# Optimization experiments

Hardware: AMD Instinct MI355X
Metric: run time of the kernel (lower is better)

The kernel has to match this reference:

```python
import jax, jax.numpy as jnp
import numpy as np

B = 2
SEQ = 384            # args.seq_len (per-stock sub-sequence length)
N_AUX = 4            # len(args.aux_tickers)
S = SEQ * N_AUX + 1  # global separator token + tiled sub-sequences
D_MODEL = 512
NHEAD = 8
HEAD_DIM = 64
ROPE = 32            # qk_rope_dim
KV_C = 256
Q_C = 384
D_FF = 1536
H2 = NHEAD * 2       # differential attention sub-heads
DH = HEAD_DIM // 2
RH = ROPE // 2
EPS = 1.1920929e-07  # torch RMSNorm default eps (fp32 machine eps)
SCALING = 1.0 / ((HEAD_DIM + ROPE) // 2)
LAMBDA_INIT = 0.8 - 0.6 * float(np.exp(-0.3 * 0))  # depth=0 -> 0.2


def rmsnorm(x, w, eps=EPS):
    return x * jax.lax.rsqrt(jnp.mean(jnp.square(x), -1, keepdims=True) + eps) * w


def apply_rope(xs, cos, sin):
    # xs: [B, N_AUX, SEQ, H2, RH]; cos/sin: [SEQ, RH//2]
    xr = xs[..., 0::2]
    xi = xs[..., 1::2]
    c = cos[None, None, :, None, :]
    s = sin[None, None, :, None, :]
    yr = xr * c - xi * s
    yi = xr * s + xi * c
    return jnp.stack([yr, yi], axis=-1).reshape(xs.shape)


def _build_mask():
    causal = np.triu(np.ones((SEQ, SEQ), np.bool_), 1)
    tiled = np.tile(causal, (N_AUX, N_AUX))
    m = np.ones((S, S), np.bool_)
    m[:, 0] = False          # everyone attends to global separator
    m[1:, 1:] = tiled
    return jnp.asarray(m)[None, None]  # [1,1,S,S], True = masked


MASK = _build_mask()


def setup_inputs() -> dict:
    key = jax.random.key(0)
    ks = jax.random.split(key, 16)

    def w(k, shape, std=0.02):
        return jax.random.normal(k, shape, jnp.float32) * std

    x = jax.random.normal(ks[0], (B, S, D_MODEL), jnp.float32)
    # rope table: complex [SEQ, ROPE//4] stored as (cos, sin)
    pairs = ROPE // 4
    inv = 1.0 / (10000.0 ** (np.arange(pairs, dtype=np.float64) / pairs))
    ang = np.outer(np.arange(SEQ), inv)
    freqs = jnp.asarray(np.stack([np.cos(ang), np.sin(ang)], -1), jnp.float32)
    return {
        'x': x,
        'freqs': freqs,
        'W_kv_down': w(ks[1], (D_MODEL, KV_C + ROPE)),
        'W_q_down': w(ks[2], (D_MODEL, Q_C)),
        'W_kv_up': w(ks[3], (KV_C, NHEAD * HEAD_DIM * 2)),
        'W_q_up': w(ks[4], (Q_C, NHEAD * (HEAD_DIM + ROPE))),
        'kv_norm_w': jnp.ones((KV_C,), jnp.float32),
        'q_norm_w': jnp.ones((Q_C,), jnp.float32),
        'W_o': w(ks[5], (NHEAD * HEAD_DIM, D_MODEL)),
        'lambda_q1': w(ks[6], (DH,), 0.1),
        'lambda_k1': w(ks[7], (DH,), 0.1),
        'lambda_q2': w(ks[8], (DH,), 0.1),
        'lambda_k2': w(ks[9], (DH,), 0.1),
        'head_norm_w': jnp.ones((HEAD_DIM,), jnp.float32),
        'norm1_w': jnp.ones((D_MODEL,), jnp.float32),
        'norm2_w': jnp.ones((D_MODEL,), jnp.float32),
        'W_ff_in': w(ks[10], (D_MODEL, 2 * D_FF)),
        'W_ff_out': w(ks[11], (D_FF, D_MODEL)),
    }


def reference(x, freqs, W_kv_down, W_q_down, W_kv_up, W_q_up, kv_norm_w, q_norm_w,
              W_o, lambda_q1, lambda_k1, lambda_q2, lambda_k2, head_norm_w,
              norm1_w, norm2_w, W_ff_in, W_ff_out):
    cos, sin = freqs[..., 0], freqs[..., 1]
    # ---- attention block (pre-norm) ----
    h = rmsnorm(x, norm1_w)
    ckv_full = h @ W_kv_down                               # [B,S,KV_C+ROPE]
    c_kv, k_rope = ckv_full[..., :KV_C], ckv_full[..., KV_C:]
    kv = (rmsnorm(c_kv, kv_norm_w) @ W_kv_up).reshape(B, S, NHEAD, 2 * HEAD_DIM)
    k, v = kv[..., :HEAD_DIM], kv[..., HEAD_DIM:]
    k = k.reshape(B, S, H2, DH)
    qf = (rmsnorm(h @ W_q_down, q_norm_w) @ W_q_up).reshape(B, S, NHEAD, HEAD_DIM + ROPE)
    q, q_rope = qf[..., :HEAD_DIM], qf[..., HEAD_DIM:]
    q = q.reshape(B, S, H2, DH)
    k_rope = jnp.broadcast_to(k_rope[:, :, None, :], (B, S, NHEAD, ROPE)).reshape(B, S, H2, RH)
    q_rope = q_rope.reshape(B, S, H2, RH)
    # split off global separator token, rope per sub-sequence
    q_sep, q_rot = q_rope[:, :1], q_rope[:, 1:].reshape(B, N_AUX, SEQ, H2, RH)
    k_sep, k_rot = k_rope[:, :1], k_rope[:, 1:].reshape(B, N_AUX, SEQ, H2, RH)
    q_rot = apply_rope(q_rot, cos, sin).reshape(B, S - 1, H2, RH)
    k_rot = apply_rope(k_rot, cos, sin).reshape(B, S - 1, H2, RH)
    q_rope = jnp.concatenate([q_sep, q_rot], axis=1)
    k_rope = jnp.concatenate([k_sep, k_rot], axis=1)
    qh = jnp.concatenate([q, q_rope], -1).transpose(0, 2, 1, 3)  # [B,H2,S,DH+RH]
    kh = jnp.concatenate([k, k_rope], -1).transpose(0, 2, 1, 3)
    a = jnp.einsum('bhqd,bhkd->bhqk', qh, kh) * SCALING
    abs_a = jnp.where(MASK, -1e9, jnp.abs(a))
    p = jnp.sign(a) * jax.nn.softmax(abs_a, axis=-1)
    lam = (jnp.exp(jnp.sum(lambda_q1 * lambda_k1)) -
           jnp.exp(jnp.sum(lambda_q2 * lambda_k2)) + LAMBDA_INIT)
    p = p.reshape(B, NHEAD, 2, S, S)
    G = jnp.mean(p[:, :, 0], axis=-1, keepdims=True)
    att = p[:, :, 0] - lam * p[:, :, 1] + G * lam
    att = jnp.where(MASK, 0.0, att)
    o = jnp.einsum('bhqk,bkhd->bqhd', att, v)              # [B,S,NHEAD,HEAD_DIM]
    o = rmsnorm(o, head_norm_w, 1e-5).reshape(B, S, NHEAD * HEAD_DIM)
    x = x + o @ W_o
    # ---- SwiGLU FFN ----
    h2 = rmsnorm(x, norm2_w)
    uv = h2 @ W_ff_in
    u, g = uv[..., :D_FF], uv[..., D_FF:]
    return x + (u * jax.nn.silu(g)) @ W_ff_out
```

## Files before the change

### kernel.cpp

```cpp
#include <hip/hip_runtime.h>

#define NB 2
#define SEQN 384
#define NS 1537
#define NS_PAD 1600
#define NH 8
#define H2N 16
#define NM (NB*NS)
#define DFF 1536
#define EPS1 1.1920929e-07f
#define SCAL (1.0f/48.0f)
#define SC2 (SCAL * 1.4426950408889634f)

#define SWZ(row, col) ((((row) << 6)) + ((col) ^ (((row) & 7) << 3)))

typedef __bf16 bf16x8 __attribute__((ext_vector_type(8)));
typedef _Float16 f16x8 __attribute__((ext_vector_type(8)));
typedef float f32x4 __attribute__((ext_vector_type(4)));

__device__ __forceinline__ unsigned short f2bf(float f) {
    unsigned int u = __builtin_bit_cast(unsigned int, f);
    u += 0x7FFFu + ((u >> 16) & 1u);
    return (unsigned short)(u >> 16);
}
__device__ __forceinline__ float bf2f(unsigned short h) {
    unsigned int u = ((unsigned int)h) << 16;
    return __builtin_bit_cast(float, u);
}

__host__ __device__ inline void tile_info(int t, int& nb0, int& nbc, int& w, int& nch) {
    int lo = (t == 0) ? 1 : t * 64;
    int hi0 = t * 64 + 63;
    int hi = hi0 < NS - 1 ? hi0 : NS - 1;
    int maxpos = ((lo - 1) / SEQN != (hi - 1) / SEQN) ? (SEQN - 1) : (hi - 1) % SEQN;
    nb0 = (maxpos + 65) >> 6;
    nbc = (maxpos + 64) >> 6;
    w = nb0 + 3 * nbc;
    nch = (w + 6) / 7;
}

struct TD { const float* w; unsigned short* hi; unsigned short* lo; int K; int N; int perm; };
struct TD7 { TD d[7]; int tend[7]; };

__global__ __launch_bounds__(256) void transpose_all(TD7 a) {
    __shared__ float tile[32][33];
    int t = blockIdx.x;
    int i = 0;
    while (t >= a.tend[i]) i++;
    int base = (i == 0) ? 0 : a.tend[i - 1];
    int lt = t - base;
    const float* w = a.d[i].w;
    unsigned short* hi = a.d[i].hi;
    unsigned short* lo = a.d[i].lo;
    int K = a.d[i].K, N = a.d[i].N, perm = a.d[i].perm;
    int Nh = N >> 1;
    int kt = (K + 31) / 32;
    int k0 = (lt % kt) * 32, n0 = (lt / kt) * 32;
    int tx = threadIdx.x & 31, ty4 = (threadIdx.x >> 5) * 4;
    for (int q = 0; q < 4; q++) {
        int k = k0 + ty4 + q, n = n0 + tx;
        tile[ty4 + q][tx] = (k < K && n < N) ? w[(size_t)k * N + n] : 0.f;
// ... 55 lines not shown
    float v0 = xx[288 + tid];
    float v1 = (tid < 128) ? xx[288 + 256 + tid] : 0.f;
    float ss2 = v0 * v0 + v1 * v1;
    for (int o = 1; o < 64; o <<= 1) ss2 += __shfl_xor(ss2, o);
    if ((tid & 63) == 0) red[tid >> 6] = ss2;
    __syncthreads();
    tot = red[0] + red[1] + red[2] + red[3];
    rs = rsqrtf(tot / 384.f + EPS1);
    float yb = v0 * rs * wB[tid];
    hb = f2bf(yb);
    bh_[(size_t)row * 384 + tid] = hb;
    bl_[(size_t)row * 384 + tid] = f2bf(yb - bf2f(hb));
    if (tid < 128) {
        float yc = v1 * rs * wB[256 + tid];
        unsigned short hc = f2bf(yc);
        bh_[(size_t)row * 384 + 256 + tid] = hc;
        bl_[(size_t)row * 384 + 256 + tid] = f2bf(yc - bf2f(hc));
    }
}

__global__ __launch_bounds__(256) void gemm_single(const unsigned short* __restrict__ A,
    const unsigned short* __restrict__ Bt, float* __restrict__ C_, const float* __restrict__ res,
    int M, int N, int K) {
    __shared__ unsigned short As[128][32];
    __shared__ unsigned short Bs[64][32];
    int m0 = blockIdx.x * 128, n0 = blockIdx.y * 64;
    int tid = threadIdx.x;
    int lane = tid & 63, wid = tid >> 6;
    int wr = wid >> 1, wc = wid & 1;
    int r = lane & 15, g = lane >> 4;
    int lrow = tid >> 2, lk = (tid & 3) * 8;
    f32x4 acc[4][2] = {};
    int ar0 = m0 + lrow, ar1 = m0 + 64 + lrow, brow = n0 + lrow;
    bool a0ok = ar0 < M, a1ok = ar1 < M, bok = brow < N;
    size_t a0off = (size_t)ar0 * K + lk, a1off = (size_t)ar1 * K + lk, boff = (size_t)brow * K + lk;
    for (int k0 = 0; k0 < K; k0 += 32) {
        uint4 av0 = {0,0,0,0}, av1 = {0,0,0,0}, bv = {0,0,0,0};
        if (a0ok) av0 = *(const uint4*)(A + a0off + k0);
        if (a1ok) av1 = *(const uint4*)(A + a1off + k0);
        if (bok)  bv  = *(const uint4*)(Bt + boff + k0);
        __syncthreads();
        *(uint4*)&As[lrow][lk] = av0;
        *(uint4*)&As[64 + lrow][lk] = av1;
        *(uint4*)&Bs[lrow][lk] = bv;
        __syncthreads();
        bf16x8 a[4], bb[2];
        #pragma unroll
        for (int i = 0; i < 4; i++) a[i] = *(const bf16x8*)&As[wr * 64 + i * 16 + r][g * 8];
        #pragma unroll
        for (int j = 0; j < 2; j++) bb[j] = *(const bf16x8*)&Bs[wc * 32 + j * 16 + r][g * 8];
        #pragma unroll
        for (int i = 0; i < 4; i++)
            #pragma unroll
            for (int j = 0; j < 2; j++)
                acc[i][j] = __builtin_amdgcn_mfma_f32_16x16x32_bf16(a[i], bb[j], acc[i][j], 0, 0, 0);
    }
    #pragma unroll
    for (int i = 0; i < 4; i++)
        #pragma unroll
        for (int j = 0; j < 2; j++) {
            int col = n0 + wc * 32 + j * 16 + r;
            if (col >= N) continue;
            #pragma unroll
            for (int e = 0; e < 4; e++) {
                int row = m0 + wr * 64 + i * 16 + g * 4 + e;
                if (row >= M) continue;
                float v = acc[i][j][e];
                if (res) v += res[(size_t)row * N + col];
                C_[(size_t)row * N + col] = v;
            }
        }
}

__global__ __launch_bounds__(256) void gemm_swiglu(const unsigned short* __restrict__ A,
    const unsigned short* __restrict__ Bt, unsigned short* __restrict__ act,
    int M, int N, int K) {
    __shared__ unsigned short As[128][32];
    __shared__ unsigned short Bs[64][32];
    int m0 = blockIdx.x * 128, n0 = blockIdx.y * 64;
    int tid = threadIdx.x;
    int lane = tid & 63, wid = tid >> 6;
    int wr = wid >> 1, wc = wid & 1;
    int r = lane & 15, g = lane >> 4;
    int lrow = tid >> 2, lk = (tid & 3) * 8;
    f32x4 acc[4][2] = {};
    int ar0 = m0 + lrow, ar1 = m0 + 64 + lrow, brow = n0 + lrow;
    bool a0ok = ar0 < M, a1ok = ar1 < M, bok = brow < N;
    size_t a0off = (size_t)ar0 * K + lk, a1off = (size_t)ar1 * K + lk, boff = (size_t)brow * K + lk;
    for (int k0 = 0; k0 < K; k0 += 32) {
        uint4 av0 = {0,0,0,0}, av1 = {0,0,0,0}, bv = {0,0,0,0};
        if (a0ok) av0 = *(const uint4*)(A + a0off + k0);
        if (a1ok) av1 = *(const uint4*)(A + a1off + k0);
        if (bok)  bv  = *(const uint4*)(Bt + boff + k0);
        __syncthreads();
        *(uint4*)&As[lrow][lk] = av0;
        *(uint4*)&As[64 + lrow][lk] = av1;
        *(uint4*)&Bs[lrow][lk] = bv;
        __syncthreads();
        bf16x8 a[4], bb[2];
        #pragma unroll
        for (int i = 0; i < 4; i++) a[i] = *(const bf16x8*)&As[wr * 64 + i * 16 + r][g * 8];
        #pragma unroll
        for (int j = 0; j < 2; j++) bb[j] = *(const bf16x8*)&Bs[wc * 32 + j * 16 + r][g * 8];
        #pragma unroll
        for (int i = 0; i < 4; i++)
            #pragma unroll
            for (int j = 0; j < 2; j++)
                acc[i][j] = __builtin_amdgcn_mfma_f32_16x16x32_bf16(a[i], bb[j], acc[i][j], 0, 0, 0);
    }
    int Nh = N >> 1;
    #pragma unroll
    for (int i = 0; i < 4; i++)
        #pragma unroll
        for (int j = 0; j < 2; j++) {
            int col = n0 + wc * 32 + j * 16 + r;
            #pragma unroll
            for (int e = 0; e < 4; e++) {
                int row = m0 + wr * 64 + i * 16 + g * 4 + e;
                float v = acc[i][j][e];
                float o = __shfl_xor(v, 1);
                if (((r & 1) == 0) && row < M && col < N) {
                    float u = v, gg = o;
                    float sg = gg / (1.f + __expf(-gg));
                    act[(size_t)row * Nh + (col >> 1)] = f2bf(u * sg);
                }
            }
        }
}

__global__ __launch_bounds__(256) void gemm_x3(const unsigned short* __restrict__ Ah,
    const unsigned short* __restrict__ Al, const unsigned short* __restrict__ Bh,
    const unsigned short* __restrict__ Bl, float* __restrict__ C_, int M, int N, int K) {
    __shared__ unsigned short AsH[128][32], AsL[128][32], BsH[64][32], BsL[64][32];
    int m0 = blockIdx.x * 128, n0 = blockIdx.y * 64;
    int tid = threadIdx.x;
    int lane = tid & 63, wid = tid >> 6;
    int wr = wid >> 1, wc = wid & 1;
    int r = lane & 15, g = lane >> 4;
    int lrow = tid >> 2, lk = (tid & 3) * 8;
    f32x4 acc[4][2] = {};
    int ar0 = m0 + lrow, ar1 = m0 + 64 + lrow, brow = n0 + lrow;
    bool a0ok = ar0 < M, a1ok = ar1 < M, bok = brow < N;
    size_t a0off = (size_t)ar0 * K + lk, a1off = (size_t)ar1 * K + lk, boff = (size_t)brow * K + lk;
    for (int k0 = 0; k0 < K; k0 += 32) {
        uint4 ah0 = {0,0,0,0}, al0 = {0,0,0,0}, ah1 = {0,0,0,0}, al1 = {0,0,0,0};
        uint4 bh0 = {0,0,0,0}, bl0 = {0,0,0,0};
        if (a0ok) { ah0 = *(const uint4*)(Ah + a0off + k0); al0 = *(const uint4*)(Al + a0off + k0); }
        if (a1ok) { ah1 = *(const uint4*)(Ah + a1off + k0); al1 = *(const uint4*)(Al + a1off + k0); }
        if (bok)  { bh0 = *(const uint4*)(Bh + boff + k0);  bl0 = *(const uint4*)(Bl + boff + k0); }
        __syncthreads();
        *(uint4*)&AsH[lrow][lk] = ah0; *(uint4*)&AsH[64 + lrow][lk] = ah1;
        *(uint4*)&AsL[lrow][lk] = al0; *(uint4*)&AsL[64 + lrow][lk] = al1;
        *(uint4*)&BsH[lrow][lk] = bh0; *(uint4*)&BsL[lrow][lk] = bl0;
        __syncthreads();
        bf16x8 ah[4], al[4], bh[2], bl[2];
        #pragma unroll
        for (int i = 0; i < 4; i++) {
            ah[i] = *(const bf16x8*)&AsH[wr * 64 + i * 16 + r][g * 8];
            al[i] = *(const bf16x8*)&AsL[wr * 64 + i * 16 + r][g * 8];
        }
        #pragma unroll
        for (int j = 0; j < 2; j++) {
            bh[j] = *(const bf16x8*)&BsH[wc * 32 + j * 16 + r][g * 8];
            bl[j] = *(const bf16x8*)&BsL[wc * 32 + j * 16 + r][g * 8];
        }
        #pragma unroll
        for (int i = 0; i < 4; i++)
            #pragma unroll
            for (int j = 0; j < 2; j++) {
                acc[i][j] = __builtin_amdgcn_mfma_f32_16x16x32_bf16(al[i], bh[j], acc[i][j], 0, 0, 0);
                acc[i][j] = __builtin_amdgcn_mfma_f32_16x16x32_bf16(ah[i], bl[j], acc[i][j], 0, 0, 0);
                acc[i][j] = __builtin_amdgcn_mfma_f32_16x16x32_bf16(ah[i], bh[j], acc[i][j], 0, 0, 0);
            }
    }
    #pragma unroll
    for (int i = 0; i < 4; i++)
        #pragma unroll
        for (int j = 0; j < 2; j++) {
            int col = n0 + wc * 32 + j * 16 + r;
            if (col >= N) continue;
            #pragma unroll
            for (int e = 0; e < 4; e++) {
                int row = m0 + wr * 64 + i * 16 + g * 4 + e;
                if (row < M) C_[(size_t)row * N + col] = acc[i][j][e];
            }
        }
}

__global__ void assemble2(const float* __restrict__ qf_, const float* __restrict__ kvf,
    const float* __restrict__ cq, const float* __restrict__ freqs,
    _Float16* __restrict__ qgh, _Float16* __restrict__ qgl,
    _Float16* __restrict__ kgh, _Float16* __restrict__ kgl) {
    size_t idx = (size_t)blockIdx.x * 256 + threadIdx.x;
    const size_t total = (size_t)NB * H2N * NS_PAD * 32;
    if (idx >= total) return;
    int j2 = (int)(idx & 31);
// ... 58 lines not shown
    int bh = blockIdx.x; int b = bh >> 3, h = bh & 7;
    int d = threadIdx.x & 63, ps = threadIdx.x >> 6;
    int p0 = ps * 96;
    float run = 0.f;
    for (int i = 0; i < 96; i++) {
        int p = p0 + i;
        float s = 0.f;
        #pragma unroll
        for (int c = 0; c < 4; c++)
            s += kvf[((size_t)(b * NS + 1 + c * SEQN + p)) * 1024 + h * 128 + 64 + d];
        run += s;
        P4[((size_t)bh * SEQN + p) * 64 + d] = run;
    }
    tot[ps][d] = run;
    __syncthreads();
    if (ps > 0) {
        float off = 0.f;
        for (int j = 0; j < ps; j++) off += tot[j][d];
        for (int i = 0; i < 96; i++)
            P4[((size_t)bh * SEQN + p0 + i) * 64 + d] += off;
    }
}

struct FlashTab { int4 e[80]; };

__global__ __launch_bounds__(256) void flash_chunk(
    const _Float16* __restrict__ qgh, const _Float16* __restrict__ qgl,
    const _Float16* __restrict__ kgh, const _Float16* __restrict__ kgl,
    const _Float16* __restrict__ vt,
    float* __restrict__ Opart, float* __restrict__ zpart, FlashTab tab) {
    __shared__ _Float16 Ksh[2][64 * 64];
    __shared__ _Float16 Ksl[2][64 * 64];
    __shared__ _Float16 Vt[64 * 64];
    __shared__ _Float16 Pl[4][16 * 64];
    const int4 E = tab.e[blockIdx.x];
    const int tq = E.x, kti0 = E.y, nk = E.z, slot = E.w;
    const int bh = blockIdx.y;
    const int b = bh >> 3, h = bh & 7;
    const int qs0 = tq * 64;
    const int tid = threadIdx.x;
    const int wave = tid >> 6, lane = tid & 63;
    const int r = lane & 15, g = lane >> 4;
    const int qrow = qs0 + wave * 16;
    const size_t sh0 = (size_t)(bh * 2);

    int nb0, nbc, w_, nch_;
    tile_info(tq, nb0, nbc, w_, nch_);

    f16x8 qfh[2][2], qfl[2][2];
    #pragma unroll
    for (int sub = 0; sub < 2; sub++)
        #pragma unroll
        for (int ks = 0; ks < 2; ks++) {
            size_t off = ((sh0 + sub) * NS_PAD + qrow + r) * 64 + ks * 32 + g * 8;
            qfh[sub][ks] = *(const f16x8*)(qgh + off);
            qfl[sub][ks] = *(const f16x8*)(qgl + off);
        }

    float z0p[4] = {0.f,0.f,0.f,0.f}, g0p[4] = {0.f,0.f,0.f,0.f}, z1p[4] = {0.f,0.f,0.f,0.f};
    f32x4 O0[4], O1[4];
    #pragma unroll
    for (int e = 0; e < 4; e++) { O0[e] = (f32x4){0.f,0.f,0.f,0.f}; O1[e] = (f32x4){0.f,0.f,0.f,0.f}; }
    int qpos[4];
    #pragma unroll
    for (int e = 0; e < 4; e++) {
        int q = qrow + g * 4 + e;
        qpos[e] = (q == 0) ? -1 : (q - 1) % SEQN;
    }

    for (int ii = 0; ii < nk; ii++) {
        int kti = kti0 + ii;
        int c, j;
        if (kti < nb0) { c = 0; j = kti; }
        else { int m = kti - nb0; c = 1 + m / nbc; j = m - (c - 1) * nbc; }
        int kbase = (c == 0) ? j * 64 : c * SEQN + 1 + j * 64;
        int cbase = c * SEQN + 1;
        __syncthreads();
        #pragma unroll
        for (int i = 0; i < 4; i++) {
            int chunk = i * 256 + tid;
            int arr = chunk >> 9;
            int cc = chunk & 511;
            int row = cc >> 3, c8 = (cc & 7) * 8;
            size_t goff = ((sh0 + arr) * NS_PAD + kbase + row) * 64 + c8;
            int di = SWZ(row, c8);
            *(uint4*)&Ksh[arr][di] = *(const uint4*)(kgh + goff);
            *(uint4*)&Ksl[arr][di] = *(const uint4*)(kgl + goff);
        }
        #pragma unroll
        for (int i = 0; i < 2; i++) {
            int cc = i * 256 + tid;
            int d = cc >> 3, c8 = (cc & 7) * 8;
            *(uint4*)&Vt[SWZ(d, c8)] =
                *(const uint4*)(vt + ((size_t)(bh * 64 + d)) * NS_PAD + kbase + c8);
        }
        __syncthreads();

        f16x8 bv[4][2];
        #pragma unroll
        for (int dt = 0; dt < 4; dt++)
            #pragma unroll
            for (int ks = 0; ks < 2; ks++)
                bv[dt][ks] = *(const f16x8*)&Vt[SWZ(dt * 16 + r, ks * 32 + g * 8)];

        bool um[4][4];
        #pragma unroll
        for (int t4 = 0; t4 < 4; t4++) {
            int kk2 = kbase + t4 * 16 + r;
            int rel = kk2 - cbase;
            #pragma unroll
            for (int e = 0; e < 4; e++)
                um[e][t4] = (kk2 == 0) ||
                            ((unsigned)rel < (unsigned)SEQN && rel <= qpos[e]);
        }

        #pragma unroll
        for (int sub = 0; sub < 2; sub++) {
            f32x4 acc[4];
            #pragma unroll
            for (int t4 = 0; t4 < 4; t4++) acc[t4] = (f32x4){0.f,0.f,0.f,0.f};
            #pragma unroll
            for (int t4 = 0; t4 < 4; t4++)
                #pragma unroll
                for (int ks = 0; ks < 2; ks++) {
                    int ki = SWZ(t4 * 16 + r, ks * 32 + g * 8);
                    f16x8 bkh = *(const f16x8*)&Ksh[sub][ki];
                    f16x8 bkl = *(const f16x8*)&Ksl[sub][ki];
                    acc[t4] = __builtin_amdgcn_mfma_f32_16x16x32_f16(qfl[sub][ks], bkh, acc[t4], 0, 0, 0);
                    acc[t4] = __builtin_amdgcn_mfma_f32_16x16x32_f16(qfh[sub][ks], bkl, acc[t4], 0, 0, 0);
                    acc[t4] = __builtin_amdgcn_mfma_f32_16x16x32_f16(qfh[sub][ks], bkh, acc[t4], 0, 0, 0);
                }
            #pragma unroll
            for (int e = 0; e < 4; e++) {
                #pragma unroll
                for (int t4 = 0; t4 < 4; t4++) {
                    float a = acc[t4][e];
                    float ef = exp2f(fabsf(a) * SC2);
                    float ev = um[e][t4] ? ef : 0.f;
                    float pvv = copysignf(ev, a);
                    if (sub == 0) { z0p[e] += ev; g0p[e] += pvv; }
                    else          { z1p[e] += ev; }
                    Pl[wave][SWZ(g * 4 + e, t4 * 16 + r)] = (_Float16)pvv;
                }
            }
            __builtin_amdgcn_wave_barrier();
            f16x8 pa0 = *(const f16x8*)&Pl[wave][SWZ(r, g * 8)];
            f16x8 pa1 = *(const f16x8*)&Pl[wave][SWZ(r, 32 + g * 8)];
            #pragma unroll
            for (int dt = 0; dt < 4; dt++) {
                if (sub == 0) {
                    O0[dt] = __builtin_amdgcn_mfma_f32_16x16x32_f16(pa0, bv[dt][0], O0[dt], 0, 0, 0);
                    O0[dt] = __builtin_amdgcn_mfma_f32_16x16x32_f16(pa1, bv[dt][1], O0[dt], 0, 0, 0);
                } else {
                    O1[dt] = __builtin_amdgcn_mfma_f32_16x16x32_f16(pa0, bv[dt][0], O1[dt], 0, 0, 0);
                    O1[dt] = __builtin_amdgcn_mfma_f32_16x16x32_f16(pa1, bv[dt][1], O1[dt], 0, 0, 0);
                }
            }
        }
    }

    #pragma unroll
    for (int e = 0; e < 4; e++) {
        float z0 = z0p[e], g0 = g0p[e], z1 = z1p[e];
        #pragma unroll
        for (int o = 1; o < 16; o <<= 1) {
            z0 += __shfl_xor(z0, o); g0 += __shfl_xor(g0, o); z1 += __shfl_xor(z1, o);
        }
        int q = qrow + g * 4 + e;
        if (q < NS) {
            if (r == 0) {
                float* zp = zpart + (((size_t)slot * 16 + bh) * NS + q) * 4;
                zp[0] = z0; zp[1] = g0; zp[2] = z1;
            }
            float* op = Opart + (((size_t)slot * 16 + bh) * NS + q) * 128;
            #pragma unroll
            for (int dt = 0; dt < 4; dt++) {
                op[dt * 16 + r] = O0[dt][e];
                op[64 + dt * 16 + r] = O1[dt][e];
            }
        }
    }
}

__global__ __launch_bounds__(256) void combine_attn(const float* __restrict__ Opart,
    const float* __restrict__ zpart, const float* __restrict__ kvf,
    const float* __restrict__ P4,
    const float* __restrict__ lq1, const float* __restrict__ lk1,
    const float* __restrict__ lq2, const float* __restrict__ lk2,
    const float* __restrict__ hw, unsigned short* __restrict__ o_n) {
    __shared__ float lamS;
    if (threadIdx.x < 32) {
        float p1 = lq1[threadIdx.x] * lk1[threadIdx.x];
        float p2 = lq2[threadIdx.x] * lk2[threadIdx.x];
        for (int o = 1; o < 32; o <<= 1) { p1 += __shfl_xor(p1, o); p2 += __shfl_xor(p2, o); }
        if (threadIdx.x == 0) lamS = expf(p1) - expf(p2) + 0.2f;
    }
    __syncthreads();
    float lam = lamS;
    int b = blockIdx.z, h = blockIdx.y, bh = b * 8 + h;
    int ql = threadIdx.x >> 2, dp = threadIdx.x & 3;
    int q = blockIdx.x * 64 + ql;
    bool ok = q < NS;
    int qc = ok ? q : 0;
    int tq = qc >> 6;
    int nb0_, nbc_, w_, nch;
    tile_info(tq, nb0_, nbc_, w_, nch);
    float z0 = 0.f, g0 = 0.f, z1 = 0.f;
    float O0a[16], O1a[16];
    #pragma unroll
    for (int i = 0; i < 16; i++) { O0a[i] = 0.f; O1a[i] = 0.f; }
    for (int s = 0; s < nch; s++) {
        size_t ib = ((size_t)s * 16 + bh) * NS + qc;
        const float* zp = zpart + ib * 4;
        z0 += zp[0]; g0 += zp[1]; z1 += zp[2];
        const float* op = Opart + ib * 128 + dp * 16;
        #pragma unroll
        for (int i = 0; i < 16; i++) { O0a[i] += op[i]; O1a[i] += op[64 + i]; }
    }
    float iz0 = 1.f / z0;
    float l1 = lam / z1;
    float Gl = lam * g0 * iz0 * (1.f / (float)NS);
    int qpos = (q == 0) ? -1 : (q - 1) % SEQN;
    float of[16]; float ss = 0.f;
    #pragma unroll
    for (int i = 0; i < 16; i++) {
        int d = dp * 16 + i;
        float vs = kvf[((size_t)(b * NS)) * 1024 + h * 128 + 64 + d];
        if (qpos >= 0) vs += P4[((size_t)bh * SEQN + qpos) * 64 + d];
        float o = O0a[i] * iz0 - O1a[i] * l1 + Gl * vs;
        of[i] = o; ss += o * o;
    }
    ss += __shfl_xor(ss, 1); ss += __shfl_xor(ss, 2);
    float rs = rsqrtf(ss / 64.f + 1e-5f);
    if (ok) {
        unsigned int pk[8];
        #pragma unroll
        for (int i = 0; i < 8; i++) {
            unsigned int a = f2bf(of[2 * i] * rs * hw[dp * 16 + 2 * i]);
            unsigned int c = f2bf(of[2 * i + 1] * rs * hw[dp * 16 + 2 * i + 1]);
            pk[i] = a | (c << 16);
        }
        unsigned short* dst = o_n + ((size_t)(b * NS + q)) * 512 + h * 64 + dp * 16;
        *(uint4*)dst = *(uint4*)&pk[0];
        *(uint4*)(dst + 8) = *(uint4*)&pk[4];
    }
}

extern "C" void kernel_launch(void* const* d_in, const int* in_sizes, int n_in,
                              void* d_out, int out_size, void* d_ws, size_t ws_size,
                              hipStream_t stream) {
    (void)in_sizes; (void)n_in; (void)out_size; (void)ws_size;
    const float* x    = (const float*)d_in[0];
// ... 30 lines not shown
    unsigned short* wffi_h = (unsigned short*)alloc((size_t)512 * 3072 * 2);
    unsigned short* wffo_h = (unsigned short*)alloc((size_t)1536 * 512 * 2);
    unsigned short* h_hi   = (unsigned short*)alloc((size_t)NM * 512 * 2);
    unsigned short* h_lo   = (unsigned short*)alloc((size_t)NM * 512 * 2);
    char* cq0 = p;
    float* cq = (float*)alloc((size_t)NM * 672 * 4);
    float* x2 = (float*)cq0;
    char* nb0_ = p;
    unsigned short* ckvn_h = (unsigned short*)alloc((size_t)NM * 256 * 2);
    unsigned short* ckvn_l = (unsigned short*)alloc((size_t)NM * 256 * 2);
    unsigned short* qdn_h  = (unsigned short*)alloc((size_t)NM * 384 * 2);
    unsigned short* qdn_l  = (unsigned short*)alloc((size_t)NM * 384 * 2);
    unsigned short* o_n    = (unsigned short*)alloc((size_t)NM * 512 * 2);
    unsigned short* h2     = (unsigned short*)alloc((size_t)NM * 512 * 2);
    unsigned short* act    = (unsigned short*)nb0_;
    float* kvf = (float*)alloc((size_t)NM * 1024 * 4);
    float* qff = (float*)alloc((size_t)NM * 768 * 4);
    _Float16* qgh = (_Float16*)alloc((size_t)NB * H2N * NS_PAD * 64 * 2);
    _Float16* qgl = (_Float16*)alloc((size_t)NB * H2N * NS_PAD * 64 * 2);
    _Float16* kgh = (_Float16*)alloc((size_t)NB * H2N * NS_PAD * 64 * 2);
    _Float16* kgl = (_Float16*)alloc((size_t)NB * H2N * NS_PAD * 64 * 2);
    _Float16* vt  = (_Float16*)alloc((size_t)NB * NH * 64 * NS_PAD * 2);
    float* P4     = (float*)alloc((size_t)NB * NH * SEQN * 64 * 4);
    float* Opart  = (float*)alloc((size_t)4 * 16 * NS * 128 * 4);
    float* zpart  = (float*)alloc((size_t)4 * 16 * NS * 4 * 4);

    int cum = 0;
    {
        TD7 a;
        const float* ws_[7] = {Wkvd, Wqd, Wkvu, Wqu, Wo, Wffi, Wffo};
        unsigned short* his[7] = {wcq_h, wcq_h + (size_t)288 * 512, wkvu_h, wqu_h, wo_h, wffi_h, wffo_h};
        unsigned short* los[7] = {wcq_l, wcq_l + (size_t)288 * 512, wkvu_l, wqu_l, nullptr, nullptr, nullptr};
        int Ks[7] = {512, 512, 256, 384, 512, 512, 1536};
        int Ns[7] = {288, 384, 1024, 768, 512, 3072, 512};
        int pm[7] = {0, 0, 0, 0, 0, 1, 0};
        for (int i = 0; i < 7; i++) {
            a.d[i] = TD{ws_[i], his[i], los[i], Ks[i], Ns[i], pm[i]};
            cum += ((Ks[i] + 31) / 32) * ((Ns[i] + 31) / 32);
            a.tend[i] = cum;
        }
        transpose_all<<<dim3(cum), 256, 0, stream>>>(a);
    }

    rmsnorm_k<<<NM, 256, 0, stream>>>(x, n1w, h_hi, h_lo, 512, 512, EPS1);

    const int GX = (NM + 127) / 128;
    gemm_x3<<<dim3(GX, (672 + 63) / 64), 256, 0, stream>>>(h_hi, h_lo, wcq_h, wcq_l, cq, NM, 672, 512);

    rmsnorm_dual<<<NM, 256, 0, stream>>>(cq, kvnw, qnw, ckvn_h, ckvn_l, qdn_h, qdn_l);

    gemm_x3<<<dim3(GX, 1024 / 64), 256, 0, stream>>>(ckvn_h, ckvn_l, wkvu_h, wkvu_l, kvf, NM, 1024, 256);
    gemm_x3<<<dim3(GX, 768 / 64), 256, 0, stream>>>(qdn_h, qdn_l, wqu_h, wqu_l, qff, NM, 768, 384);

    {
        size_t total = (size_t)NB * H2N * NS_PAD * 32;
        assemble2<<<dim3((unsigned)((total + 255) / 256)), 256, 0, stream>>>(
            qff, kvf, cq, freqs, qgh, qgl, kgh, kgl);
    }
    vtrans<<<dim3(NS_PAD / 64, NB * NH), 256, 0, stream>>>(kvf, vt);
    prefix2_k<<<dim3(NB * NH), 256, 0, stream>>>(kvf, P4);

    {
        FlashTab tab;
        int ne = 0;
        for (int t = 0; t < (NS + 63) / 64; t++) {
            int nb0c, nbcc, w, nch;
            tile_info(t, nb0c, nbcc, w, nch);
            int base = 0;
            for (int i = 0; i < nch; i++) {
                int sz = w / nch + (i < w % nch ? 1 : 0);
                tab.e[ne++] = make_int4(t, base, sz, i);
                base += sz;
            }
        }
        for (int i = 1; i < ne; i++) {
            int4 key = tab.e[i];
            int j = i - 1;
            while (j >= 0 && tab.e[j].z < key.z) { tab.e[j + 1] = tab.e[j]; j--; }
            tab.e[j + 1] = key;
        }
        flash_chunk<<<dim3(ne, 16), 256, 0, stream>>>(qgh, qgl, kgh, kgl, vt, Opart, zpart, tab);
    }
    combine_attn<<<dim3((NS + 63) / 64, NH, NB), 256, 0, stream>>>(
        Opart, zpart, kvf, P4, lq1, lk1, lq2, lk2, hnw, o_n);

    gemm_single<<<dim3(GX, 512 / 64), 256, 0, stream>>>(o_n, wo_h, x2, x, NM, 512, 512);
    rmsnorm_k<<<NM, 256, 0, stream>>>(x2, n2w, h2, nullptr, 512, 512, EPS1);
    gemm_swiglu<<<dim3(GX, 3072 / 64), 256, 0, stream>>>(h2, wffi_h, act, NM, 3072, 512);
    gemm_single<<<dim3(GX, 512 / 64), 256, 0, stream>>>(act, wffo_h, out, x2, NM, 512, 1536);
}
```

Before: 311.7 us.

## Widen GEMM K-tiles with swizzled LDS and replace chunked flash table with fixed 2-way split

All three GEMM kernels now stage 64-wide K slices in XOR-swizzled shared memory instead of 32-wide padded-free arrays. This halves the number of barrier pairs per K loop and avoids LDS bank conflicts. The attention kernel drops the host-built work table of load-balanced chunks in favour of a fixed split into two halves over the four sub-sequences, adding s_setprio around the MFMA blocks. The combine kernel now sums exactly two partials. The fixed split may balance load worse than the sorted chunk table, and the bigger tiles use more LDS, which can lower occupancy.

```diff
diff --git a/kernel.cpp b/kernel.cpp
--- a/kernel.cpp
+++ b/kernel.cpp
@@ -26,17 +26,6 @@
 __device__ __forceinline__ float bf2f(unsigned short h) {
     unsigned int u = ((unsigned int)h) << 16;
     return __builtin_bit_cast(float, u);
-}
-
-__host__ __device__ inline void tile_info(int t, int& nb0, int& nbc, int& w, int& nch) {
-    int lo = (t == 0) ? 1 : t * 64;
-    int hi0 = t * 64 + 63;
-    int hi = hi0 < NS - 1 ? hi0 : NS - 1;
-    int maxpos = ((lo - 1) / SEQN != (hi - 1) / SEQN) ? (SEQN - 1) : (hi - 1) % SEQN;
-    nb0 = (maxpos + 65) >> 6;
-    nbc = (maxpos + 64) >> 6;
-    w = nb0 + 3 * nbc;
-    nch = (w + 6) / 7;
 }
 
 struct TD { const float* w; unsigned short* hi; unsigned short* lo; int K; int N; int perm; };
@@ -138,38 +127,54 @@
 __global__ __launch_bounds__(256) void gemm_single(const unsigned short* __restrict__ A,
     const unsigned short* __restrict__ Bt, float* __restrict__ C_, const float* __restrict__ res,
     int M, int N, int K) {
-    __shared__ unsigned short As[128][32];
-    __shared__ unsigned short Bs[64][32];
+    __shared__ unsigned short As[128 * 64];
+    __shared__ unsigned short Bs[64 * 64];
     int m0 = blockIdx.x * 128, n0 = blockIdx.y * 64;
     int tid = threadIdx.x;
     int lane = tid & 63, wid = tid >> 6;
     int wr = wid >> 1, wc = wid & 1;
     int r = lane & 15, g = lane >> 4;
-    int lrow = tid >> 2, lk = (tid & 3) * 8;
+    int lrow = tid >> 3, lk = (tid & 7) * 8;
     f32x4 acc[4][2] = {};
-    int ar0 = m0 + lrow, ar1 = m0 + 64 + lrow, brow = n0 + lrow;
-    bool a0ok = ar0 < M, a1ok = ar1 < M, bok = brow < N;
-    size_t a0off = (size_t)ar0 * K + lk, a1off = (size_t)ar1 * K + lk, boff = (size_t)brow * K + lk;
-    for (int k0 = 0; k0 < K; k0 += 32) {
-        uint4 av0 = {0,0,0,0}, av1 = {0,0,0,0}, bv = {0,0,0,0};
-        if (a0ok) av0 = *(const uint4*)(A + a0off + k0);
-        if (a1ok) av1 = *(const uint4*)(A + a1off + k0);
-        if (bok)  bv  = *(const uint4*)(Bt + boff + k0);
+    bool aok[4]; size_t aoff[4];
+    #pragma unroll
+    for (int p = 0; p < 4; p++) {
+        int ar = m0 + p * 32 + lrow;
+        aok[p] = ar < M;
+        aoff[p] = (size_t)ar * K + lk;
+    }
+    bool bok[2]; size_t boff[2];
+    #pragma unroll
+    for (int p = 0; p < 2; p++) {
+        int br = n0 + p * 32 + lrow;
+        bok[p] = br < N;
+        boff[p] = (size_t)br * K + lk;
+    }
+    for (int k0 = 0; k0 < K; k0 += 64) {
+        uint4 av[4], bv[2];
+        #pragma unroll
+        for (int p = 0; p < 4; p++) av[p] = aok[p] ? *(const uint4*)(A + aoff[p] + k0) : (uint4){0,0,0,0};
+        #pragma unroll
+        for (int p = 0; p < 2; p++) bv[p] = bok[p] ? *(const uint4*)(Bt + boff[p] + k0) : (uint4){0,0,0,0};
         __syncthreads();
-        *(uint4*)&As[lrow][lk] = av0;
-        *(uint4*)&As[64 + lrow][lk] = av1;
-        *(uint4*)&Bs[lrow][lk] = bv;
+        #pragma unroll
+        for (int p = 0; p < 4; p++) *(uint4*)&As[SWZ(p * 32 + lrow, lk)] = av[p];
+        #pragma unroll
+        for (int p = 0; p < 2; p++) *(uint4*)&Bs[SWZ(p * 32 + lrow, lk)] = bv[p];
         __syncthreads();
-        bf16x8 a[4], bb[2];
-        #pragma unroll
-        for (int i = 0; i < 4; i++) a[i] = *(const bf16x8*)&As[wr * 64 + i * 16 + r][g * 8];
-        #pragma unroll
-        for (int j = 0; j < 2; j++) bb[j] = *(const bf16x8*)&Bs[wc * 32 + j * 16 + r][g * 8];
-        #pragma unroll
-        for (int i = 0; i < 4; i++)
-            #pragma unroll
-            for (int j = 0; j < 2; j++)
-                acc[i][j] = __builtin_amdgcn_mfma_f32_16x16x32_bf16(a[i], bb[j], acc[i][j], 0, 0, 0);
+        #pragma unroll
+        for (int ks = 0; ks < 2; ks++) {
+            bf16x8 a[4], bb[2];
+            #pragma unroll
+            for (int i = 0; i < 4; i++) a[i] = *(const bf16x8*)&As[SWZ(wr * 64 + i * 16 + r, ks * 32 + g * 8)];
+            #pragma unroll
+            for (int j = 0; j < 2; j++) bb[j] = *(const bf16x8*)&Bs[SWZ(wc * 32 + j * 16 + r, ks * 32 + g * 8)];
+            #pragma unroll
+            for (int i = 0; i < 4; i++)
+                #pragma unroll
+                for (int j = 0; j < 2; j++)
+                    acc[i][j] = __builtin_amdgcn_mfma_f32_16x16x32_bf16(a[i], bb[j], acc[i][j], 0, 0, 0);
+        }
     }
     #pragma unroll
     for (int i = 0; i < 4; i++)
@@ -191,38 +196,54 @@
 __global__ __launch_bounds__(256) void gemm_swiglu(const unsigned short* __restrict__ A,
     const unsigned short* __restrict__ Bt, unsigned short* __restrict__ act,
     int M, int N, int K) {
-    __shared__ unsigned short As[128][32];
-    __shared__ unsigned short Bs[64][32];
+    __shared__ unsigned short As[128 * 64];
+    __shared__ unsigned short Bs[64 * 64];
     int m0 = blockIdx.x * 128, n0 = blockIdx.y * 64;
     int tid = threadIdx.x;
     int lane = tid & 63, wid = tid >> 6;
     int wr = wid >> 1, wc = wid & 1;
     int r = lane & 15, g = lane >> 4;
-    int lrow = tid >> 2, lk = (tid & 3) * 8;
+    int lrow = tid >> 3, lk = (tid & 7) * 8;
     f32x4 acc[4][2] = {};
-    int ar0 = m0 + lrow, ar1 = m0 + 64 + lrow, brow = n0 + lrow;
-    bool a0ok = ar0 < M, a1ok = ar1 < M, bok = brow < N;
-    size_t a0off = (size_t)ar0 * K + lk, a1off = (size_t)ar1 * K + lk, boff = (size_t)brow * K + lk;
-    for (int k0 = 0; k0 < K; k0 += 32) {
-        uint4 av0 = {0,0,0,0}, av1 = {0,0,0,0}, bv = {0,0,0,0};
-        if (a0ok) av0 = *(const uint4*)(A + a0off + k0);
-        if (a1ok) av1 = *(const uint4*)(A + a1off + k0);
-        if (bok)  bv  = *(const uint4*)(Bt + boff + k0);
+    bool aok[4]; size_t aoff[4];
+    #pragma unroll
+    for (int p = 0; p < 4; p++) {
+        int ar = m0 + p * 32 + lrow;
+        aok[p] = ar < M;
+        aoff[p] = (size_t)ar * K + lk;
+    }
+    bool bok[2]; size_t boff[2];
+    #pragma unroll
+    for (int p = 0; p < 2; p++) {
+        int br = n0 + p * 32 + lrow;
+        bok[p] = br < N;
+        boff[p] = (size_t)br * K + lk;
+    }
+    for (int k0 = 0; k0 < K; k0 += 64) {
+        uint4 av[4], bv[2];
+        #pragma unroll
+        for (int p = 0; p < 4; p++) av[p] = aok[p] ? *(const uint4*)(A + aoff[p] + k0) : (uint4){0,0,0,0};
+        #pragma unroll
+        for (int p = 0; p < 2; p++) bv[p] = bok[p] ? *(const uint4*)(Bt + boff[p] + k0) : (uint4){0,0,0,0};
         __syncthreads();
-        *(uint4*)&As[lrow][lk] = av0;
-        *(uint4*)&As[64 + lrow][lk] = av1;
-        *(uint4*)&Bs[lrow][lk] = bv;
+        #pragma unroll
+        for (int p = 0; p < 4; p++) *(uint4*)&As[SWZ(p * 32 + lrow, lk)] = av[p];
+        #pragma unroll
+        for (int p = 0; p < 2; p++) *(uint4*)&Bs[SWZ(p * 32 + lrow, lk)] = bv[p];
         __syncthreads();
-        bf16x8 a[4], bb[2];
-        #pragma unroll
-        for (int i = 0; i < 4; i++) a[i] = *(const bf16x8*)&As[wr * 64 + i * 16 + r][g * 8];
-        #pragma unroll
-        for (int j = 0; j < 2; j++) bb[j] = *(const bf16x8*)&Bs[wc * 32 + j * 16 + r][g * 8];
-        #pragma unroll
-        for (int i = 0; i < 4; i++)
-            #pragma unroll
-            for (int j = 0; j < 2; j++)
-                acc[i][j] = __builtin_amdgcn_mfma_f32_16x16x32_bf16(a[i], bb[j], acc[i][j], 0, 0, 0);
+        #pragma unroll
+        for (int ks = 0; ks < 2; ks++) {
+            bf16x8 a[4], bb[2];
+            #pragma unroll
+            for (int i = 0; i < 4; i++) a[i] = *(const bf16x8*)&As[SWZ(wr * 64 + i * 16 + r, ks * 32 + g * 8)];
+            #pragma unroll
+            for (int j = 0; j < 2; j++) bb[j] = *(const bf16x8*)&Bs[SWZ(wc * 32 + j * 16 + r, ks * 32 + g * 8)];
+            #pragma unroll
+            for (int i = 0; i < 4; i++)
+                #pragma unroll
+                for (int j = 0; j < 2; j++)
+                    acc[i][j] = __builtin_amdgcn_mfma_f32_16x16x32_bf16(a[i], bb[j], acc[i][j], 0, 0, 0);
+        }
     }
     int Nh = N >> 1;
     #pragma unroll
@@ -247,47 +268,76 @@
 __global__ __launch_bounds__(256) void gemm_x3(const unsigned short* __restrict__ Ah,
     const unsigned short* __restrict__ Al, const unsigned short* __restrict__ Bh,
     const unsigned short* __restrict__ Bl, float* __restrict__ C_, int M, int N, int K) {
-    __shared__ unsigned short AsH[128][32], AsL[128][32], BsH[64][32], BsL[64][32];
+    __shared__ unsigned short AsH[128 * 64], AsL[128 * 64], BsH[64 * 64], BsL[64 * 64];
     int m0 = blockIdx.x * 128, n0 = blockIdx.y * 64;
     int tid = threadIdx.x;
     int lane = tid & 63, wid = tid >> 6;
     int wr = wid >> 1, wc = wid & 1;
     int r = lane & 15, g = lane >> 4;
-    int lrow = tid >> 2, lk = (tid & 3) * 8;
+    int lrow = tid >> 3, lk = (tid & 7) * 8;
     f32x4 acc[4][2] = {};
-    int ar0 = m0 + lrow, ar1 = m0 + 64 + lrow, brow = n0 + lrow;
-    bool a0ok = ar0 < M, a1ok = ar1 < M, bok = brow < N;
-    size_t a0off = (size_t)ar0 * K + lk, a1off = (size_t)ar1 * K + lk, boff = (size_t)brow * K + lk;
-    for (int k0 = 0; k0 < K; k0 += 32) {
-        uint4 ah0 = {0,0,0,0}, al0 = {0,0,0,0}, ah1 = {0,0,0,0}, al1 = {0,0,0,0};
-        uint4 bh0 = {0,0,0,0}, bl0 = {0,0,0,0};
-        if (a0ok) { ah0 = *(const uint4*)(Ah + a0off + k0); al0 = *(const uint4*)(Al + a0off + k0); }
-        if (a1ok) { ah1 = *(const uint4*)(Ah + a1off + k0); al1 = *(const uint4*)(Al + a1off + k0); }
-        if (bok)  { bh0 = *(const uint4*)(Bh + boff + k0);  bl0 = *(const uint4*)(Bl + boff + k0); }
+    bool aok[4]; size_t aoff[4];
+    #pragma unroll
+    for (int p = 0; p < 4; p++) {
+        int ar = m0 + p * 32 + lrow;
+        aok[p] = ar < M;
+        aoff[p] = (size_t)ar * K + lk;
+    }
+    bool bok[2]; size_t boff[2];
+    #pragma unroll
+    for (int p = 0; p < 2; p++) {
+        int br = n0 + p * 32 + lrow;
+        bok[p] = br < N;
+        boff[p] = (size_t)br * K + lk;
+    }
+    for (int k0 = 0; k0 < K; k0 += 64) {
+        uint4 avh[4], avl[4], bvh[2], bvl[2];
+        #pragma unroll
+        for (int p = 0; p < 4; p++) {
+            avh[p] = aok[p] ? *(const uint4*)(Ah + aoff[p] + k0) : (uint4){0,0,0,0};
+            avl[p] = aok[p] ? *(const uint4*)(Al + aoff[p] + k0) : (uint4){0,0,0,0};
+        }
+        #pragma unroll
+        for (int p = 0; p < 2; p++) {
+            bvh[p] = bok[p] ? *(const uint4*)(Bh + boff[p] + k0) : (uint4){0,0,0,0};
+            bvl[p] = bok[p] ? *(const uint4*)(Bl + boff[p] + k0) : (uint4){0,0,0,0};
+        }
         __syncthreads();
-        *(uint4*)&AsH[lrow][lk] = ah0; *(uint4*)&AsH[64 + lrow][lk] = ah1;
-        *(uint4*)&AsL[lrow][lk] = al0; *(uint4*)&AsL[64 + lrow][lk] = al1;
-        *(uint4*)&BsH[lrow][lk] = bh0; *(uint4*)&BsL[lrow][lk] = bl0;
+        #pragma unroll
+        for (int p = 0; p < 4; p++) {
+            *(uint4*)&AsH[SWZ(p * 32 + lrow, lk)] = avh[p];
+            *(uint4*)&AsL[SWZ(p * 32 + lrow, lk)] = avl[p];
+        }
+        #pragma unroll
+        for (int p = 0; p < 2; p++) {
+            *(uint4*)&BsH[SWZ(p * 32 + lrow, lk)] = bvh[p];
+            *(uint4*)&BsL[SWZ(p * 32 + lrow, lk)] = bvl[p];
+        }
         __syncthreads();
-        bf16x8 ah[4], al[4], bh[2], bl[2];
-        #pragma unroll
-        for (int i = 0; i < 4; i++) {
-            ah[i] = *(const bf16x8*)&AsH[wr * 64 + i * 16 + r][g * 8];
-            al[i] = *(const bf16x8*)&AsL[wr * 64 + i * 16 + r][g * 8];
-        }
-        #pragma unroll
-        for (int j = 0; j < 2; j++) {
-            bh[j] = *(const bf16x8*)&BsH[wc * 32 + j * 16 + r][g * 8];
-            bl[j] = *(const bf16x8*)&BsL[wc * 32 + j * 16 + r][g * 8];
-        }
-        #pragma unroll
-        for (int i = 0; i < 4; i++)
+        #pragma unroll
+        for (int ks = 0; ks < 2; ks++) {
+            bf16x8 ah[4], al[4], bh[2], bl[2];
+            #pragma unroll
+            for (int i = 0; i < 4; i++) {
+                int ai = SWZ(wr * 64 + i * 16 + r, ks * 32 + g * 8);
+                ah[i] = *(const bf16x8*)&AsH[ai];
+                al[i] = *(const bf16x8*)&AsL[ai];
+            }
             #pragma unroll
             for (int j = 0; j < 2; j++) {
-                acc[i][j] = __builtin_amdgcn_mfma_f32_16x16x32_bf16(al[i], bh[j], acc[i][j], 0, 0, 0);
-                acc[i][j] = __builtin_amdgcn_mfma_f32_16x16x32_bf16(ah[i], bl[j], acc[i][j], 0, 0, 0);
-                acc[i][j] = __builtin_amdgcn_mfma_f32_16x16x32_bf16(ah[i], bh[j], acc[i][j], 0, 0, 0);
-            }
+                int bi = SWZ(wc * 32 + j * 16 + r, ks * 32 + g * 8);
+                bh[j] = *(const bf16x8*)&BsH[bi];
+                bl[j] = *(const bf16x8*)&BsL[bi];
+            }
+            #pragma unroll
+            for (int i = 0; i < 4; i++)
+                #pragma unroll
+                for (int j = 0; j < 2; j++) {
+                    acc[i][j] = __builtin_amdgcn_mfma_f32_16x16x32_bf16(al[i], bh[j], acc[i][j], 0, 0, 0);
+                    acc[i][j] = __builtin_amdgcn_mfma_f32_16x16x32_bf16(ah[i], bl[j], acc[i][j], 0, 0, 0);
+                    acc[i][j] = __builtin_amdgcn_mfma_f32_16x16x32_bf16(ah[i], bh[j], acc[i][j], 0, 0, 0);
+                }
+        }
     }
     #pragma unroll
     for (int i = 0; i < 4; i++)
@@ -392,31 +442,26 @@
     }
 }
 
-struct FlashTab { int4 e[80]; };
-
-__global__ __launch_bounds__(256) void flash_chunk(
+__global__ __launch_bounds__(256) void flash_split(
     const _Float16* __restrict__ qgh, const _Float16* __restrict__ qgl,
     const _Float16* __restrict__ kgh, const _Float16* __restrict__ kgl,
     const _Float16* __restrict__ vt,
-    float* __restrict__ Opart, float* __restrict__ zpart, FlashTab tab) {
+    float* __restrict__ Opart, float* __restrict__ zpart) {
     __shared__ _Float16 Ksh[2][64 * 64];
     __shared__ _Float16 Ksl[2][64 * 64];
     __shared__ _Float16 Vt[64 * 64];
     __shared__ _Float16 Pl[4][16 * 64];
-    const int4 E = tab.e[blockIdx.x];
-    const int tq = E.x, kti0 = E.y, nk = E.z, slot = E.w;
-    const int bh = blockIdx.y;
-    const int b = bh >> 3, h = bh & 7;
-    const int qs0 = tq * 64;
+    const int tile = blockIdx.x;
+    const int h = blockIdx.y & 7, split = blockIdx.y >> 3;
+    const int b = blockIdx.z;
+    const int bh = b * 8 + h;
+    const int qs0 = tile * 64;
     const int tid = threadIdx.x;
     const int wave = tid >> 6, lane = tid & 63;
     const int r = lane & 15, g = lane >> 4;
     const int qrow = qs0 + wave * 16;
     const size_t sh0 = (size_t)(bh * 2);
 
-    int nb0, nbc, w_, nch_;
-    tile_info(tq, nb0, nbc, w_, nch_);
-
     f16x8 qfh[2][2], qfl[2][2];
     #pragma unroll
     for (int sub = 0; sub < 2; sub++)
@@ -437,94 +482,101 @@
         int q = qrow + g * 4 + e;
         qpos[e] = (q == 0) ? -1 : (q - 1) % SEQN;
     }
-
-    for (int ii = 0; ii < nk; ii++) {
-        int kti = kti0 + ii;
-        int c, j;
-        if (kti < nb0) { c = 0; j = kti; }
-        else { int m = kti - nb0; c = 1 + m / nbc; j = m - (c - 1) * nbc; }
-        int kbase = (c == 0) ? j * 64 : c * SEQN + 1 + j * 64;
+    int lo = qs0 < 1 ? 1 : qs0;
+    int hi = qs0 + 63 < NS - 1 ? qs0 + 63 : NS - 1;
+    int maxpos = ((lo - 1) / SEQN != (hi - 1) / SEQN) ? (SEQN - 1) : (hi - 1) % SEQN;
+
+    for (int c = 2 * split; c < 2 * split + 2; c++) {
+        int nb = (c == 0) ? ((maxpos + 2 + 63) >> 6) : ((maxpos + 1 + 63) >> 6);
+        int kstart = (c == 0) ? 0 : (c * SEQN + 1);
         int cbase = c * SEQN + 1;
-        __syncthreads();
-        #pragma unroll
-        for (int i = 0; i < 4; i++) {
-            int chunk = i * 256 + tid;
-            int arr = chunk >> 9;
-            int cc = chunk & 511;
-            int row = cc >> 3, c8 = (cc & 7) * 8;
-            size_t goff = ((sh0 + arr) * NS_PAD + kbase + row) * 64 + c8;
-            int di = SWZ(row, c8);
-            *(uint4*)&Ksh[arr][di] = *(const uint4*)(kgh + goff);
-            *(uint4*)&Ksl[arr][di] = *(const uint4*)(kgl + goff);
-        }
-        #pragma unroll
-        for (int i = 0; i < 2; i++) {
-            int cc = i * 256 + tid;
-            int d = cc >> 3, c8 = (cc & 7) * 8;
-            *(uint4*)&Vt[SWZ(d, c8)] =
-                *(const uint4*)(vt + ((size_t)(bh * 64 + d)) * NS_PAD + kbase + c8);
-        }
-        __syncthreads();
-
-        f16x8 bv[4][2];
-        #pragma unroll
-        for (int dt = 0; dt < 4; dt++)
-            #pragma unroll
-            for (int ks = 0; ks < 2; ks++)
-                bv[dt][ks] = *(const f16x8*)&Vt[SWZ(dt * 16 + r, ks * 32 + g * 8)];
-
-        bool um[4][4];
-        #pragma unroll
-        for (int t4 = 0; t4 < 4; t4++) {
-            int kk2 = kbase + t4 * 16 + r;
-            int rel = kk2 - cbase;
-            #pragma unroll
-            for (int e = 0; e < 4; e++)
-                um[e][t4] = (kk2 == 0) ||
-                            ((unsigned)rel < (unsigned)SEQN && rel <= qpos[e]);
-        }
-
-        #pragma unroll
-        for (int sub = 0; sub < 2; sub++) {
-            f32x4 acc[4];
-            #pragma unroll
-            for (int t4 = 0; t4 < 4; t4++) acc[t4] = (f32x4){0.f,0.f,0.f,0.f};
-            #pragma unroll
-            for (int t4 = 0; t4 < 4; t4++)
-                #pragma unroll
-                for (int ks = 0; ks < 2; ks++) {
-                    int ki = SWZ(t4 * 16 + r, ks * 32 + g * 8);
-                    f16x8 bkh = *(const f16x8*)&Ksh[sub][ki];
-                    f16x8 bkl = *(const f16x8*)&Ksl[sub][ki];
-                    acc[t4] = __builtin_amdgcn_mfma_f32_16x16x32_f16(qfl[sub][ks], bkh, acc[t4], 0, 0, 0);
-                    acc[t4] = __builtin_amdgcn_mfma_f32_16x16x32_f16(qfh[sub][ks], bkl, acc[t4], 0, 0, 0);
-                    acc[t4] = __builtin_amdgcn_mfma_f32_16x16x32_f16(qfh[sub][ks], bkh, acc[t4], 0, 0, 0);
+        for (int j = 0; j < nb; j++) {
+            int kbase = kstart + j * 64;
+            __syncthreads();
+            #pragma unroll
+            for (int i = 0; i < 4; i++) {
+                int chunk = i * 256 + tid;
+                int arr = chunk >> 9;
+                int cc = chunk & 511;
+                int row = cc >> 3, c8 = (cc & 7) * 8;
+                size_t goff = ((sh0 + arr) * NS_PAD + kbase + row) * 64 + c8;
+                int di = SWZ(row, c8);
+                *(uint4*)&Ksh[arr][di] = *(const uint4*)(kgh + goff);
+                *(uint4*)&Ksl[arr][di] = *(const uint4*)(kgl + goff);
+            }
+            #pragma unroll
+            for (int i = 0; i < 2; i++) {
+                int cc = i * 256 + tid;
+                int d = cc >> 3, c8 = (cc & 7) * 8;
+                *(uint4*)&Vt[SWZ(d, c8)] =
+                    *(const uint4*)(vt + ((size_t)(bh * 64 + d)) * NS_PAD + kbase + c8);
+            }
+            __syncthreads();
+
+            f16x8 bv[4][2];
+            #pragma unroll
+            for (int dt = 0; dt < 4; dt++)
+                #pragma unroll
+                for (int ks = 0; ks < 2; ks++)
+                    bv[dt][ks] = *(const f16x8*)&Vt[SWZ(dt * 16 + r, ks * 32 + g * 8)];
+
+            bool um[4][4];
+            #pragma unroll
+            for (int t4 = 0; t4 < 4; t4++) {
+                int kk2 = kbase + t4 * 16 + r;
+                int rel = kk2 - cbase;
+                #pragma unroll
+                for (int e = 0; e < 4; e++)
+                    um[e][t4] = (kk2 == 0) ||
+                                ((unsigned)rel < (unsigned)SEQN && rel <= qpos[e]);
+            }
+
+            #pragma unroll
+            for (int sub = 0; sub < 2; sub++) {
+                f32x4 acc[4];
+                #pragma unroll
+                for (int t4 = 0; t4 < 4; t4++) acc[t4] = (f32x4){0.f,0.f,0.f,0.f};
+                __builtin_amdgcn_s_setprio(1);
+                #pragma unroll
+                for (int t4 = 0; t4 < 4; t4++)
+                    #pragma unroll
+                    for (int ks = 0; ks < 2; ks++) {
+                        int ki = SWZ(t4 * 16 + r, ks * 32 + g * 8);
+                        f16x8 bkh = *(const f16x8*)&Ksh[sub][ki];
+                        f16x8 bkl = *(const f16x8*)&Ksl[sub][ki];
+                        acc[t4] = __builtin_amdgcn_mfma_f32_16x16x32_f16(qfl[sub][ks], bkh, acc[t4], 0, 0, 0);
+                        acc[t4] = __builtin_amdgcn_mfma_f32_16x16x32_f16(qfh[sub][ks], bkl, acc[t4], 0, 0, 0);
+                        acc[t4] = __builtin_amdgcn_mfma_f32_16x16x32_f16(qfh[sub][ks], bkh, acc[t4], 0, 0, 0);
+                    }
+                __builtin_amdgcn_s_setprio(0);
+                #pragma unroll
+                for (int e = 0; e < 4; e++) {
+                    #pragma unroll
+                    for (int t4 = 0; t4 < 4; t4++) {
+                        float a = acc[t4][e];
+                        float ef = exp2f(fabsf(a) * SC2);
+                        float ev = um[e][t4] ? ef : 0.f;
+                        float pvv = copysignf(ev, a);
+                        if (sub == 0) { z0p[e] += ev; g0p[e] += pvv; }
+                        else          { z1p[e] += ev; }
+                        Pl[wave][SWZ(g * 4 + e, t4 * 16 + r)] = (_Float16)pvv;
+                    }
                 }
-            #pragma unroll
-            for (int e = 0; e < 4; e++) {
-                #pragma unroll
-                for (int t4 = 0; t4 < 4; t4++) {
-                    float a = acc[t4][e];
-                    float ef = exp2f(fabsf(a) * SC2);
-                    float ev = um[e][t4] ? ef : 0.f;
-                    float pvv = copysignf(ev, a);
-                    if (sub == 0) { z0p[e] += ev; g0p[e] += pvv; }
-                    else          { z1p[e] += ev; }
-                    Pl[wave][SWZ(g * 4 + e, t4 * 16 + r)] = (_Float16)pvv;
+                __builtin_amdgcn_wave_barrier();
+                f16x8 pa0 = *(const f16x8*)&Pl[wave][SWZ(r, g * 8)];
+                f16x8 pa1 = *(const f16x8*)&Pl[wave][SWZ(r, 32 + g * 8)];
+                __builtin_amdgcn_s_setprio(1);
+                #pragma unroll
+                for (int dt = 0; dt < 4; dt++) {
+                    if (sub == 0) {
+                        O0[dt] = __builtin_amdgcn_mfma_f32_16x16x32_f16(pa0, bv[dt][0], O0[dt], 0, 0, 0);
+                        O0[dt] = __builtin_amdgcn_mfma_f32_16x16x32_f16(pa1, bv[dt][1], O0[dt], 0, 0, 0);
+                    } else {
+                        O1[dt] = __builtin_amdgcn_mfma_f32_16x16x32_f16(pa0, bv[dt][0], O1[dt], 0, 0, 0);
+                        O1[dt] = __builtin_amdgcn_mfma_f32_16x16x32_f16(pa1, bv[dt][1], O1[dt], 0, 0, 0);
+                    }
                 }
-            }
-            __builtin_amdgcn_wave_barrier();
-            f16x8 pa0 = *(const f16x8*)&Pl[wave][SWZ(r, g * 8)];
-            f16x8 pa1 = *(const f16x8*)&Pl[wave][SWZ(r, 32 + g * 8)];
-            #pragma unroll
-            for (int dt = 0; dt < 4; dt++) {
-                if (sub == 0) {
-                    O0[dt] = __builtin_amdgcn_mfma_f32_16x16x32_f16(pa0, bv[dt][0], O0[dt], 0, 0, 0);
-                    O0[dt] = __builtin_amdgcn_mfma_f32_16x16x32_f16(pa1, bv[dt][1], O0[dt], 0, 0, 0);
-                } else {
-                    O1[dt] = __builtin_amdgcn_mfma_f32_16x16x32_f16(pa0, bv[dt][0], O1[dt], 0, 0, 0);
-                    O1[dt] = __builtin_amdgcn_mfma_f32_16x16x32_f16(pa1, bv[dt][1], O1[dt], 0, 0, 0);
-                }
+                __builtin_amdgcn_s_setprio(0);
             }
         }
     }
@@ -539,10 +591,10 @@
         int q = qrow + g * 4 + e;
         if (q < NS) {
             if (r == 0) {
-                float* zp = zpart + (((size_t)slot * 16 + bh) * NS + q) * 4;
+                float* zp = zpart + (((size_t)split * 16 + bh) * NS + q) * 4;
                 zp[0] = z0; zp[1] = g0; zp[2] = z1;
             }
-            float* op = Opart + (((size_t)slot * 16 + bh) * NS + q) * 128;
+            float* op = Opart + (((size_t)split * 16 + bh) * NS + q) * 128;
             #pragma unroll
             for (int dt = 0; dt < 4; dt++) {
                 op[dt * 16 + r] = O0[dt][e];
@@ -572,32 +624,26 @@
     int q = blockIdx.x * 64 + ql;
     bool ok = q < NS;
     int qc = ok ? q : 0;
-    int tq = qc >> 6;
-    int nb0_, nbc_, w_, nch;
-    tile_info(tq, nb0_, nbc_, w_, nch);
-    float z0 = 0.f, g0 = 0.f, z1 = 0.f;
-    float O0a[16], O1a[16];
-    #pragma unroll
-    for (int i = 0; i < 16; i++) { O0a[i] = 0.f; O1a[i] = 0.f; }
-    for (int s = 0; s < nch; s++) {
-        size_t ib = ((size_t)s * 16 + bh) * NS + qc;
-        const float* zp = zpart + ib * 4;
-        z0 += zp[0]; g0 += zp[1]; z1 += zp[2];
-        const float* op = Opart + ib * 128 + dp * 16;
-        #pragma unroll
-        for (int i = 0; i < 16; i++) { O0a[i] += op[i]; O1a[i] += op[64 + i]; }
-    }
+    size_t i0 = ((size_t)0 * 16 + bh) * NS + qc;
+    size_t i1 = ((size_t)1 * 16 + bh) * NS + qc;
+    const float* za = zpart + i0 * 4;
+    const float* zb = zpart + i1 * 4;
+    float z0 = za[0] + zb[0], g0 = za[1] + zb[1], z1 = za[2] + zb[2];
     float iz0 = 1.f / z0;
     float l1 = lam / z1;
     float Gl = lam * g0 * iz0 * (1.f / (float)NS);
     int qpos = (q == 0) ? -1 : (q - 1) % SEQN;
+    const float* oa = Opart + i0 * 128 + dp * 16;
+    const float* ob = Opart + i1 * 128 + dp * 16;
     float of[16]; float ss = 0.f;
     #pragma unroll
     for (int i = 0; i < 16; i++) {
         int d = dp * 16 + i;
+        float O0 = oa[i] + ob[i];
+        float O1 = oa[64 + i] + ob[64 + i];
         float vs = kvf[((size_t)(b * NS)) * 1024 + h * 128 + 64 + d];
         if (qpos >= 0) vs += P4[((size_t)bh * SEQN + qpos) * 64 + d];
-        float o = O0a[i] * iz0 - O1a[i] * l1 + Gl * vs;
+        float o = O0 * iz0 - O1 * l1 + Gl * vs;
         of[i] = o; ss += o * o;
     }
     ss += __shfl_xor(ss, 1); ss += __shfl_xor(ss, 2);
@@ -674,8 +720,8 @@
     _Float16* kgl = (_Float16*)alloc((size_t)NB * H2N * NS_PAD * 64 * 2);
     _Float16* vt  = (_Float16*)alloc((size_t)NB * NH * 64 * NS_PAD * 2);
     float* P4     = (float*)alloc((size_t)NB * NH * SEQN * 64 * 4);
-    float* Opart  = (float*)alloc((size_t)4 * 16 * NS * 128 * 4);
-    float* zpart  = (float*)alloc((size_t)4 * 16 * NS * 4 * 4);
+    float* Opart  = (float*)alloc((size_t)2 * 16 * NS * 128 * 4);
+    float* zpart  = (float*)alloc((size_t)2 * 16 * NS * 4 * 4);
 
     int cum = 0;
     {
@@ -712,27 +758,8 @@
     vtrans<<<dim3(NS_PAD / 64, NB * NH), 256, 0, stream>>>(kvf, vt);
     prefix2_k<<<dim3(NB * NH), 256, 0, stream>>>(kvf, P4);
 
-    {
-        FlashTab tab;
-        int ne = 0;
-        for (int t = 0; t < (NS + 63) / 64; t++) {
-            int nb0c, nbcc, w, nch;
-            tile_info(t, nb0c, nbcc, w, nch);
-            int base = 0;
-            for (int i = 0; i < nch; i++) {
-                int sz = w / nch + (i < w % nch ? 1 : 0);
-                tab.e[ne++] = make_int4(t, base, sz, i);
-                base += sz;
-            }
-        }
-        for (int i = 1; i < ne; i++) {
-            int4 key = tab.e[i];
-            int j = i - 1;
-            while (j >= 0 && tab.e[j].z < key.z) { tab.e[j + 1] = tab.e[j]; j--; }
-            tab.e[j + 1] = key;
-        }
-        flash_chunk<<<dim3(ne, 16), 256, 0, stream>>>(qgh, qgl, kgh, kgl, vt, Opart, zpart, tab);
-    }
+    flash_split<<<dim3((NS + 63) / 64, 16, NB), 256, 0, stream>>>(
+        qgh, qgl, kgh, kgl, vt, Opart, zpart);
     combine_attn<<<dim3((NS + 63) / 64, NH, NB), 256, 0, stream>>>(
         Opart, zpart, kvf, P4, lq1, lk1, lq2, lk2, hnw, o_n);
 
```

Result: faster. 295.2 us (-5.3%).
